# Kernel tuning notes

Hardware: AMD Instinct MI355X
Metric: run time of the kernel (lower is better)

Reference implementation:

```python
import jax, jax.numpy as jnp
import numpy as np

B, S, D = 8, 2048, 1024


def setup_inputs() -> dict:
    key = jax.random.key(0)
    ks = jax.random.split(key, 9)
    s = 1.0 / np.sqrt(D)
    return {
        "x": jax.random.normal(ks[0], (B, S, D), dtype=jnp.float32),
        "Wq": jax.random.normal(ks[1], (D, D), dtype=jnp.float32) * s,
        "bq": jnp.zeros((D,), dtype=jnp.float32),
        "Wk": jax.random.normal(ks[2], (D, D), dtype=jnp.float32) * s,
        "bk": jnp.zeros((D,), dtype=jnp.float32),
        "Wv": jax.random.normal(ks[3], (D, D), dtype=jnp.float32) * s,
        "bv": jnp.zeros((D,), dtype=jnp.float32),
        "Wo": jax.random.normal(ks[4], (D, D), dtype=jnp.float32) * s,
        "bo": jnp.zeros((D,), dtype=jnp.float32),
    }


def reference(x, Wq, bq, Wk, bk, Wv, bv, Wo, bo):
    # Single-head self-attention with full NxN scores (as in the torch module).
    q = jnp.einsum("bsd,de->bse", x, Wq) + bq
    k = jnp.einsum("bsd,de->bse", x, Wk) + bk
    v = jnp.einsum("bsd,de->bse", x, Wv) + bv
    scores = jnp.einsum("bqd,bkd->bqk", q, k) / jnp.sqrt(jnp.float32(D))
    attn = jax.nn.softmax(scores, axis=-1)
    y = jnp.einsum("bqk,bkd->bqd", attn, v)
    return jnp.einsum("bsd,de->bse", y, Wo) + bo
```

## Files before the change

### kernel.cpp

```cpp
#include <hip/hip_runtime.h>
#include <stdint.h>


using u16 = unsigned short;
using u32 = unsigned int;
using short8  = __attribute__((ext_vector_type(8))) short;
using floatx4 = __attribute__((ext_vector_type(4))) float;

#define GPTR(p) ((__attribute__((address_space(1))) u32*)(p))
#define LPTR(p) ((__attribute__((address_space(3))) u32*)(p))

__device__ __forceinline__ void async_cp16(const void* g, void* l) {
  __builtin_amdgcn_global_load_lds(GPTR(g), LPTR(l), 16, 0, 0);
}

__device__ __forceinline__ u16 f2bf(float f) {
  u32 u = __builtin_bit_cast(u32, f);
  u = (u + 0x7fffu + ((u >> 16) & 1u)) >> 16;
  return (u16)u;
}
__device__ __forceinline__ float bf2f(u16 h) {
  u32 u = ((u32)h) << 16;
  return __builtin_bit_cast(float, u);
}

__device__ __forceinline__ void swz(int gx, int gy, int& bx, int& by) {
  int s = blockIdx.x + gx * blockIdx.y;
  int q = s >> 3;
  by = (s & 7) * (gy >> 3) + q / gx;
  bx = q % gx;
}

__device__ __forceinline__ void gemm_core(
    const u16* __restrict__ A, const u16* __restrict__ B,
    int lda, int ldb, int K, u16* lA, u16* lB, floatx4 acc[4][4])
{
  const int tid  = threadIdx.x;
  const int lane = tid & 63;
  const int w    = tid >> 6;
  const int rsub = lane >> 2;
  const int csub = lane & 3;
  const int frow = lane & 15;
  const int fq   = lane >> 4;
  const int wrow = (w >> 1) * 64;
  const int wcol = (w & 1) * 64;

  for (int k0 = 0; k0 < K; k0 += 32) {
    const u16* ga = A + (size_t)(w * 32 + rsub) * lda + k0 + csub * 8;
    async_cp16(ga,                    lA + (w * 32) * 32);
    async_cp16(ga + (size_t)16 * lda, lA + (w * 32 + 16) * 32);
    const u16* gb = B + (size_t)(w * 32 + rsub) * ldb + k0 + csub * 8;
    async_cp16(gb,                    lB + (w * 32) * 32);
    async_cp16(gb + (size_t)16 * ldb, lB + (w * 32 + 16) * 32);
    __syncthreads();

    short8 af[4], bfr[4];
#pragma unroll
    for (int i = 0; i < 4; ++i)
      af[i] = *(const short8*)(lA + (wrow + i * 16 + frow) * 32 + fq * 8);
#pragma unroll
    for (int j = 0; j < 4; ++j)
      bfr[j] = *(const short8*)(lB + (wcol + j * 16 + frow) * 32 + fq * 8);
#pragma unroll
    for (int i = 0; i < 4; ++i)
#pragma unroll
      for (int j = 0; j < 4; ++j)
        acc[i][j] = __builtin_amdgcn_mfma_f32_16x16x32_bf16(af[i], bfr[j], acc[i][j], 0, 0, 0);
    __syncthreads();
  }
}

__global__ __launch_bounds__(256) void k_cast_x(const float* __restrict__ x, u16* __restrict__ xb) {
  size_t i = ((size_t)blockIdx.x * 256 + threadIdx.x) * 8;
  float4 a = *(const float4*)(x + i);
  float4 b = *(const float4*)(x + i + 4);
  u16 o[8] __attribute__((aligned(16)));
  o[0] = f2bf(a.x); o[1] = f2bf(a.y); o[2] = f2bf(a.z); o[3] = f2bf(a.w);
  o[4] = f2bf(b.x); o[5] = f2bf(b.y); o[6] = f2bf(b.z); o[7] = f2bf(b.w);
  *(uint4*)(xb + i) = *(const uint4*)o;
}

__global__ __launch_bounds__(256) void k_cast_wt(
    const float* __restrict__ Wq, const float* __restrict__ Wk,
    const float* __restrict__ Wo, u16* __restrict__ WT)
{
  __shared__ float t[32][33];
  const int z = blockIdx.z;
  const float* W = (z == 0) ? Wq : (z == 1) ? Wk : Wo;
  u16* out = WT + (size_t)z * 1024 * 1024;
  const int c = threadIdx.x & 31, r = threadIdx.x >> 5;
#pragma unroll
  for (int p = 0; p < 4; ++p)
    t[r + 8 * p][c] = W[(size_t)(blockIdx.y * 32 + r + 8 * p) * 1024 + blockIdx.x * 32 + c];
  __syncthreads();
#pragma unroll
  for (int p = 0; p < 4; ++p)
    out[(size_t)(blockIdx.x * 32 + r + 8 * p) * 1024 + blockIdx.y * 32 + c] = f2bf(t[c][r + 8 * p]);
}

__global__ __launch_bounds__(256) void k_bvo(
    const float* __restrict__ bv, const float* __restrict__ Wo, float* __restrict__ bvo)
{
  const int nb = blockIdx.x & 3, jc = blockIdx.x >> 2;
  const int n = nb * 256 + threadIdx.x;
  float s = 0.f;
#pragma unroll 4
  for (int j = jc * 64; j < jc * 64 + 64; ++j) s += bv[j] * Wo[(size_t)j * 1024 + n];
  atomicAdd(&bvo[n], s);
}

__global__ __launch_bounds__(256) void k_wvo_part(
    const u16* __restrict__ WoT, const u16* __restrict__ Wvb, float* __restrict__ Pf)
{
  __shared__ u16 lA[4096], lB[4096];
  const int bx = blockIdx.x, by = blockIdx.y, z = blockIdx.z;
  const u16* Am = WoT + (size_t)by * 128 * 1024 + z * 256;
  const u16* Bm = Wvb + (size_t)bx * 128 * 1024 + z * 256;
  floatx4 acc[4][4] = {};
  gemm_core(Am, Bm, 1024, 1024, 256, lA, lB, acc);

  float* out = Pf + (size_t)z * 1024 * 1024;
  const int lane = threadIdx.x & 63, w = threadIdx.x >> 6;
  const int wrow = (w >> 1) * 64, wcol = (w & 1) * 64;
#pragma unroll
  for (int j = 0; j < 4; ++j) {
    const int c = bx * 128 + wcol + j * 16 + (lane & 15);
#pragma unroll
    for (int i = 0; i < 4; ++i) {
      const int m0 = by * 128 + wrow + i * 16 + (lane >> 4) * 4;
#pragma unroll
      for (int r = 0; r < 4; ++r)
        out[(size_t)(m0 + r) * 1024 + c] = acc[i][j][r];
    }
  }
}

__global__ __launch_bounds__(256) void k_wvo_red(
    const float* __restrict__ Pf, u16* __restrict__ WvoT)
{
  const size_t e = ((size_t)blockIdx.x * 256 + threadIdx.x) * 8;
  u16 o[8] __attribute__((aligned(16)));
#pragma unroll
  for (int h = 0; h < 2; ++h) {
    float4 s = *(const float4*)(Pf + e + h * 4);
#pragma unroll
    for (int z = 1; z < 4; ++z) {
      float4 p = *(const float4*)(Pf + (size_t)z * 1024 * 1024 + e + h * 4);
      s.x += p.x; s.y += p.y; s.z += p.z; s.w += p.w;
    }
    o[h * 4 + 0] = f2bf(s.x); o[h * 4 + 1] = f2bf(s.y);
    o[h * 4 + 2] = f2bf(s.z); o[h * 4 + 3] = f2bf(s.w);
  }
  *(uint4*)(WvoT + e) = *(const uint4*)o;
}

__global__ __launch_bounds__(256) void k_qkv(
    const u16* __restrict__ XB, const u16* __restrict__ WT,
    const float* __restrict__ bq, const float* __restrict__ bk, const float* __restrict__ bvo,
    u16* __restrict__ Q, u16* __restrict__ Kb, u16* __restrict__ Vt)
{
  __shared__ u16 smem[17408];
  u16* lA = smem;
  u16* lB = smem + 4096;
  int bx, by; swz(8, 128, bx, by);
  const int mode = blockIdx.z;
  const u16* Am = XB + (size_t)by * 128 * 1024;
  const int ws_idx = (mode == 2) ? 3 : mode;
  const u16* Bm = WT + (size_t)ws_idx * 1024 * 1024 + (size_t)bx * 128 * 1024;
  const float* bias = (mode == 0) ? bq : (mode == 1) ? bk : bvo;
  floatx4 acc[4][4] = {};
  gemm_core(Am, Bm, 1024, 1024, 1024, lA, lB, acc);

  const int tid = threadIdx.x, lane = tid & 63, w = tid >> 6;
  const int lane15 = lane & 15, fq = lane >> 4;
  const int wrow = (w >> 1) * 64, wcol = (w & 1) * 64;

  if (mode == 2) {
    u16* T = smem;
#pragma unroll
    for (int j = 0; j < 4; ++j) {
      const int c = wcol + j * 16 + lane15;
      const float bb = bias[bx * 128 + c];
#pragma unroll
      for (int i = 0; i < 4; ++i)
#pragma unroll
        for (int r = 0; r < 4; ++r)
          T[c * 136 + wrow + i * 16 + fq * 4 + r] = f2bf(acc[i][j][r] + bb);
    }
    __syncthreads();
    const int b = by >> 4, s0 = (by & 15) * 128, c0 = bx * 128;
#pragma unroll
    for (int kk = 0; kk < 8; ++kk) {
      const int cr = (tid >> 4) + 16 * kk, pos = tid & 15;
      uint4 val = *(const uint4*)(T + cr * 136 + pos * 8);
      *(uint4*)(Vt + ((size_t)(b * 1024 + c0 + cr)) * 2048 + s0 + pos * 8) = val;
    }
    return;
  }

#pragma unroll
  for (int j = 0; j < 4; ++j) {
    const int c = bx * 128 + wcol + j * 16 + lane15;
    const float bb = bias[c];
#pragma unroll
    for (int i = 0; i < 4; ++i) {
      const int m0 = by * 128 + wrow + i * 16 + fq * 4;
#pragma unroll
      for (int r = 0; r < 4; ++r) {
        const float v = acc[i][j][r] + bb;
        if (mode == 0) Q[(size_t)(m0 + r) * 1024 + c] = f2bf(v * 0.03125f);
        else           Kb[(size_t)(m0 + r) * 1024 + c] = f2bf(v);
      }
    }
  }
}

__global__ __launch_bounds__(256) void k_scores(
    const u16* __restrict__ Q, const u16* __restrict__ Kb, u16* __restrict__ P,
    float* __restrict__ rowsum)
{
  __shared__ u16 lA[4096], lB[4096];
  const int id = blockIdx.x;
  const int b = id & 7, rest = id >> 3;
  const int bx = rest & 15, by = rest >> 4;
  const u16* Am = Q  + (size_t)b * 2048 * 1024 + (size_t)by * 128 * 1024;
  const u16* Bm = Kb + (size_t)b * 2048 * 1024 + (size_t)bx * 128 * 1024;
  floatx4 acc[4][4] = {};
  gemm_core(Am, Bm, 1024, 1024, 1024, lA, lB, acc);

  u16* Pb = P + (size_t)b * 2048 * 2048;
  const int lane = threadIdx.x & 63, w = threadIdx.x >> 6;
  const int lane15 = lane & 15, fq = lane >> 4;
  const int wrow = (w >> 1) * 64, wcol = (w & 1) * 64;
#pragma unroll
  for (int i = 0; i < 4; ++i) {
#pragma unroll
    for (int r = 0; r < 4; ++r) {
      const int m = by * 128 + wrow + i * 16 + fq * 4 + r;
      float part = 0.f;
#pragma unroll
      for (int j = 0; j < 4; ++j) {
        const int c = bx * 128 + wcol + j * 16 + lane15;
        const float e = __expf(acc[i][j][r]);
        const u16 h = f2bf(e);
        Pb[(size_t)m * 2048 + c] = h;
        part += bf2f(h);
      }
      part += __shfl_xor(part, 1, 64);
      part += __shfl_xor(part, 2, 64);
      part += __shfl_xor(part, 4, 64);
      part += __shfl_xor(part, 8, 64);
      if (lane15 == 0) atomicAdd(&rowsum[b * 2048 + m], part);
    }
  }
}

__global__ __launch_bounds__(256) void k_pv_out(
    const u16* __restrict__ P, const u16* __restrict__ Vt,
    const float* __restrict__ bo, const float* __restrict__ rowsum,
    float* __restrict__ out)
{
  __shared__ u16 lA[4096], lB[4096];
  const int id = blockIdx.x;
  const int b = id & 7, rest = id >> 3;
  const int bx = rest & 7, by = rest >> 3;
  const u16* Am = P  + (size_t)b * 2048 * 2048 + (size_t)by * 128 * 2048;
  const u16* Bm = Vt + (size_t)b * 1024 * 2048 + (size_t)bx * 128 * 2048;
  floatx4 acc[4][4] = {};
  gemm_core(Am, Bm, 2048, 2048, 2048, lA, lB, acc);

  float* outb = out + (size_t)b * 2048 * 1024;
  const int lane = threadIdx.x & 63, w = threadIdx.x >> 6;
  const int lane15 = lane & 15, fq = lane >> 4;
  const int wrow = (w >> 1) * 64, wcol = (w & 1) * 64;
  float bb[4];
#pragma unroll
  for (int j = 0; j < 4; ++j) bb[j] = bo[bx * 128 + wcol + j * 16 + lane15];
#pragma unroll
  for (int i = 0; i < 4; ++i) {
#pragma unroll
    for (int r = 0; r < 4; ++r) {
      const int m = by * 128 + wrow + i * 16 + fq * 4 + r;
      const float inv = 1.0f / rowsum[b * 2048 + m];
#pragma unroll
      for (int j = 0; j < 4; ++j) {
        const int c = bx * 128 + wcol + j * 16 + lane15;
        outb[(size_t)m * 1024 + c] = acc[i][j][r] * inv + bb[j];
      }
    }
  }
}

extern "C" void kernel_launch(void* const* d_in, const int* in_sizes, int n_in,
                              void* d_out, int out_size, void* d_ws, size_t ws_size,
                              hipStream_t stream) {
  const float* x  = (const float*)d_in[0];
  const float* Wq = (const float*)d_in[1];
  const float* bq = (const float*)d_in[2];
  const float* Wk = (const float*)d_in[3];
  const float* bk = (const float*)d_in[4];
  const float* Wv = (const float*)d_in[5];
  const float* bv = (const float*)d_in[6];
  const float* Wo = (const float*)d_in[7];
  const float* bo = (const float*)d_in[8];
  float* out = (float*)d_out;

  char* ws = (char*)d_ws;
  u16* XB  = (u16*)(ws + 0);
  u16* WT  = (u16*)(ws + 33554432);
  u16* Q   = (u16*)(ws + 41943040);
  u16* Kb  = (u16*)(ws + 75497472);
  u16* Vt  = (u16*)(ws + 109051904);
  u16* P   = (u16*)(ws + 142606336);
  u16* Wvb = Kb;
  float* bvo    = (float*)P;
  float* WvoPf  = (float*)(ws + 142606336 + 4194304);
  float* rowsum = (float*)XB;

  if (ws_size < 209715200) return;

  k_cast_wt  <<<dim3(32, 32, 3), 256, 0, stream>>>(Wq, Wk, Wo, WT);
  k_cast_x   <<<512, 256, 0, stream>>>(Wv, Wvb);
  k_cast_x   <<<8192, 256, 0, stream>>>(x, XB);
  hipMemsetAsync(bvo, 0, 1024 * sizeof(float), stream);
  k_bvo      <<<64, 256, 0, stream>>>(bv, Wo, bvo);
  k_wvo_part <<<dim3(8, 8, 4), 256, 0, stream>>>(WT + (size_t)2 * 1024 * 1024, Wvb, WvoPf);
  k_wvo_red  <<<512, 256, 0, stream>>>(WvoPf, WT + (size_t)3 * 1024 * 1024);
  k_qkv      <<<dim3(8, 128, 3), 256, 0, stream>>>(XB, WT, bq, bk, bvo, Q, Kb, Vt);
  hipMemsetAsync(rowsum, 0, 16384 * sizeof(float), stream);
  k_scores   <<<2048, 256, 0, stream>>>(Q, Kb, P, rowsum);
  k_pv_out   <<<1024, 256, 0, stream>>>(P, Vt, bo, rowsum, out);
}
```

Measured before the change: 502.2 us.

## Double GEMM K-step to 64 with XOR-swizzled LDS layout, fold Wv cast

The shared GEMM core now loads 64-wide K slices per iteration into an XOR-swizzled LDS layout and runs two MFMA sub-steps per barrier pair, which halves the number of syncthreads and is meant to reduce LDS bank conflicts on fragment reads. LDS tiles double in size, and launch bounds now request 4 blocks per SM. The Wv bf16 cast is merged into the weight-transpose kernel as an extra z-slice, removing one launch. A barrier was added before the V-transpose epilogue reuses shared memory.

```diff
diff --git a/kernel.cpp b/kernel.cpp
--- a/kernel.cpp
+++ b/kernel.cpp
@@ -38,34 +38,46 @@
   const int tid  = threadIdx.x;
   const int lane = tid & 63;
   const int w    = tid >> 6;
-  const int rsub = lane >> 2;
-  const int csub = lane & 3;
+  const int r8   = lane >> 3;
+  const int cg   = (lane & 7) ^ r8;
   const int frow = lane & 15;
   const int fq   = lane >> 4;
   const int wrow = (w >> 1) * 64;
   const int wcol = (w & 1) * 64;
 
-  for (int k0 = 0; k0 < K; k0 += 32) {
-    const u16* ga = A + (size_t)(w * 32 + rsub) * lda + k0 + csub * 8;
-    async_cp16(ga,                    lA + (w * 32) * 32);
-    async_cp16(ga + (size_t)16 * lda, lA + (w * 32 + 16) * 32);
-    const u16* gb = B + (size_t)(w * 32 + rsub) * ldb + k0 + csub * 8;
-    async_cp16(gb,                    lB + (w * 32) * 32);
-    async_cp16(gb + (size_t)16 * ldb, lB + (w * 32 + 16) * 32);
+  const u16* gaL = A + (size_t)(w * 32 + r8) * lda + cg * 8;
+  const u16* gbL = B + (size_t)(w * 32 + r8) * ldb + cg * 8;
+  u16* lAw = lA + (w * 32) * 64;
+  u16* lBw = lB + (w * 32) * 64;
+  const int x0 = ((0 + fq) ^ (frow & 7)) * 8;
+  const int x1 = ((4 + fq) ^ (frow & 7)) * 8;
+
+  for (int k0 = 0; k0 < K; k0 += 64) {
+    const u16* ga = gaL + k0;
+    const u16* gb = gbL + k0;
+#pragma unroll
+    for (int t = 0; t < 4; ++t) {
+      async_cp16(ga + (size_t)(t * 8) * lda, lAw + t * 8 * 64);
+      async_cp16(gb + (size_t)(t * 8) * ldb, lBw + t * 8 * 64);
+    }
     __syncthreads();
 
-    short8 af[4], bfr[4];
-#pragma unroll
-    for (int i = 0; i < 4; ++i)
-      af[i] = *(const short8*)(lA + (wrow + i * 16 + frow) * 32 + fq * 8);
-#pragma unroll
-    for (int j = 0; j < 4; ++j)
-      bfr[j] = *(const short8*)(lB + (wcol + j * 16 + frow) * 32 + fq * 8);
-#pragma unroll
-    for (int i = 0; i < 4; ++i)
+#pragma unroll
+    for (int sub = 0; sub < 2; ++sub) {
+      const int xs = sub ? x1 : x0;
+      short8 af[4], bfr[4];
+#pragma unroll
+      for (int i = 0; i < 4; ++i)
+        af[i] = *(const short8*)(lA + (wrow + i * 16 + frow) * 64 + xs);
 #pragma unroll
       for (int j = 0; j < 4; ++j)
-        acc[i][j] = __builtin_amdgcn_mfma_f32_16x16x32_bf16(af[i], bfr[j], acc[i][j], 0, 0, 0);
+        bfr[j] = *(const short8*)(lB + (wcol + j * 16 + frow) * 64 + xs);
+#pragma unroll
+      for (int i = 0; i < 4; ++i)
+#pragma unroll
+        for (int j = 0; j < 4; ++j)
+          acc[i][j] = __builtin_amdgcn_mfma_f32_16x16x32_bf16(af[i], bfr[j], acc[i][j], 0, 0, 0);
+    }
     __syncthreads();
   }
 }
@@ -82,13 +94,22 @@
 
 __global__ __launch_bounds__(256) void k_cast_wt(
     const float* __restrict__ Wq, const float* __restrict__ Wk,
-    const float* __restrict__ Wo, u16* __restrict__ WT)
+    const float* __restrict__ Wo, const float* __restrict__ Wv,
+    u16* __restrict__ WT, u16* __restrict__ Wvb)
 {
   __shared__ float t[32][33];
   const int z = blockIdx.z;
+  const int c = threadIdx.x & 31, r = threadIdx.x >> 5;
+  if (z == 3) {
+#pragma unroll
+    for (int p = 0; p < 4; ++p) {
+      const size_t idx = (size_t)(blockIdx.y * 32 + r + 8 * p) * 1024 + blockIdx.x * 32 + c;
+      Wvb[idx] = f2bf(Wv[idx]);
+    }
+    return;
+  }
   const float* W = (z == 0) ? Wq : (z == 1) ? Wk : Wo;
   u16* out = WT + (size_t)z * 1024 * 1024;
-  const int c = threadIdx.x & 31, r = threadIdx.x >> 5;
 #pragma unroll
   for (int p = 0; p < 4; ++p)
     t[r + 8 * p][c] = W[(size_t)(blockIdx.y * 32 + r + 8 * p) * 1024 + blockIdx.x * 32 + c];
@@ -109,10 +130,10 @@
   atomicAdd(&bvo[n], s);
 }
 
-__global__ __launch_bounds__(256) void k_wvo_part(
+__global__ __launch_bounds__(256, 4) void k_wvo_part(
     const u16* __restrict__ WoT, const u16* __restrict__ Wvb, float* __restrict__ Pf)
 {
-  __shared__ u16 lA[4096], lB[4096];
+  __shared__ u16 lA[8192], lB[8192];
   const int bx = blockIdx.x, by = blockIdx.y, z = blockIdx.z;
   const u16* Am = WoT + (size_t)by * 128 * 1024 + z * 256;
   const u16* Bm = Wvb + (size_t)bx * 128 * 1024 + z * 256;
@@ -154,14 +175,14 @@
   *(uint4*)(WvoT + e) = *(const uint4*)o;
 }
 
-__global__ __launch_bounds__(256) void k_qkv(
+__global__ __launch_bounds__(256, 4) void k_qkv(
     const u16* __restrict__ XB, const u16* __restrict__ WT,
     const float* __restrict__ bq, const float* __restrict__ bk, const float* __restrict__ bvo,
     u16* __restrict__ Q, u16* __restrict__ Kb, u16* __restrict__ Vt)
 {
   __shared__ u16 smem[17408];
   u16* lA = smem;
-  u16* lB = smem + 4096;
+  u16* lB = smem + 8192;
   int bx, by; swz(8, 128, bx, by);
   const int mode = blockIdx.z;
   const u16* Am = XB + (size_t)by * 128 * 1024;
@@ -177,6 +198,7 @@
 
   if (mode == 2) {
     u16* T = smem;
+    __syncthreads();
 #pragma unroll
     for (int j = 0; j < 4; ++j) {
       const int c = wcol + j * 16 + lane15;
@@ -215,11 +237,11 @@
   }
 }
 
-__global__ __launch_bounds__(256) void k_scores(
+__global__ __launch_bounds__(256, 4) void k_scores(
     const u16* __restrict__ Q, const u16* __restrict__ Kb, u16* __restrict__ P,
     float* __restrict__ rowsum)
 {
-  __shared__ u16 lA[4096], lB[4096];
+  __shared__ u16 lA[8192], lB[8192];
   const int id = blockIdx.x;
   const int b = id & 7, rest = id >> 3;
   const int bx = rest & 15, by = rest >> 4;
@@ -255,12 +277,12 @@
   }
 }
 
-__global__ __launch_bounds__(256) void k_pv_out(
+__global__ __launch_bounds__(256, 4) void k_pv_out(
     const u16* __restrict__ P, const u16* __restrict__ Vt,
     const float* __restrict__ bo, const float* __restrict__ rowsum,
     float* __restrict__ out)
 {
-  __shared__ u16 lA[4096], lB[4096];
+  __shared__ u16 lA[8192], lB[8192];
   const int id = blockIdx.x;
   const int b = id & 7, rest = id >> 3;
   const int bx = rest & 7, by = rest >> 3;
@@ -319,8 +341,7 @@
 
   if (ws_size < 209715200) return;
 
-  k_cast_wt  <<<dim3(32, 32, 3), 256, 0, stream>>>(Wq, Wk, Wo, WT);
-  k_cast_x   <<<512, 256, 0, stream>>>(Wv, Wvb);
+  k_cast_wt  <<<dim3(32, 32, 4), 256, 0, stream>>>(Wq, Wk, Wo, Wv, WT, Wvb);
   k_cast_x   <<<8192, 256, 0, stream>>>(x, XB);
   hipMemsetAsync(bvo, 0, 1024 * sizeof(float), stream);
   k_bvo      <<<64, 256, 0, stream>>>(bv, Wo, bvo);
```

Result: faster. 415.0 us (-17.4%).
